# Performance work log

Hardware: AMD Instinct MI355X
Metric: run time of the kernel (lower is better)

## Reference

```python
import jax, jax.numpy as jnp
import numpy as np

B, T, D, H1, H2, O = 256, 200, 1250, 100, 20, 2
P = 0.2  # dropout prob (training=True in the original forward)


def setup_inputs() -> dict:
    key = jax.random.key(0)
    ks = jax.random.split(key, 13)
    s1 = 1.0 / np.sqrt(H1)  # torch nn.RNN init: U(-1/sqrt(hidden), 1/sqrt(hidden))
    s2 = 1.0 / np.sqrt(H2)
    sf = 1.0 / np.sqrt(H2)  # fc fan_in = 20
    u = lambda k, shape, s: jax.random.uniform(k, shape, jnp.float32, -s, s)
    keep = 1.0 - P
    return {
        "x": jax.random.normal(ks[0], (B, T, D), jnp.float32),
        "W_ih1": u(ks[1], (H1, D), s1),
        "W_hh1": u(ks[2], (H1, H1), s1),
        "b_ih1": u(ks[3], (H1,), s1),
        "b_hh1": u(ks[4], (H1,), s1),
        "W_ih2": u(ks[5], (H2, H1), s2),
        "W_hh2": u(ks[6], (H2, H2), s2),
        "b_ih2": u(ks[7], (H2,), s2),
        "b_hh2": u(ks[8], (H2,), s2),
        "W_fc": u(ks[9], (O, H2), sf),
        "b_fc": u(ks[10], (O,), sf),
        # pre-sampled inverted-dropout masks (training=True), scaled by 1/keep
        "mask1": jax.random.bernoulli(ks[11], keep, (B, T, H1)).astype(jnp.float32) / keep,
        "mask2": jax.random.bernoulli(ks[12], keep, (B, T, H2)).astype(jnp.float32) / keep,
    }


def _relu_rnn(x, W_ih, W_hh, b_ih, b_hh):
    # x: [B,T,Din] -> outputs [B,T,H]. Hoist the input projection out of the scan.
    pre = jnp.einsum("btd,hd->bth", x, W_ih) + b_ih + b_hh  # [B,T,H]
    h0 = jnp.zeros((x.shape[0], W_hh.shape[0]), x.dtype)

    def step(h, pre_t):
        h = jax.nn.relu(pre_t + h @ W_hh.T)
        return h, h

    _, out = jax.lax.scan(step, h0, jnp.swapaxes(pre, 0, 1))  # [T,B,H]
    return jnp.swapaxes(out, 0, 1)


def reference(x, W_ih1, W_hh1, b_ih1, b_hh1, W_ih2, W_hh2, b_ih2, b_hh2,
              W_fc, b_fc, mask1, mask2):
    out = _relu_rnn(x, W_ih1, W_hh1, b_ih1, b_hh1) * mask1          # rnn1 + dropout
    out = _relu_rnn(out, W_ih2, W_hh2, b_ih2, b_hh2) * mask2        # rnn2 + dropout
    return out[:, -1, :] @ W_fc.T + b_fc                            # fc on last step
```

## Files before the change

### kernel.cpp

```cpp
#include <hip/hip_runtime.h>

#define NB 256
#define TT 200
#define DD 1250
#define H1 100
#define H2 20
#define NO 2

#define BM 64
#define GRID_A (51200 / BM)
#define KC 64
#define NCH 20
#define WR 112
#define KPAD 1280

typedef __attribute__((ext_vector_type(4))) float f32x4;
typedef __attribute__((ext_vector_type(8))) short s16x8;

__device__ __forceinline__ unsigned short f2bf(float f) {
    unsigned u = __builtin_bit_cast(unsigned, f);
    u += 0x7FFFu + ((u >> 16) & 1u);
    return (unsigned short)(u >> 16);
}
__device__ __forceinline__ float bf2f(unsigned short s) {
    unsigned u = ((unsigned)s) << 16;
    return __builtin_bit_cast(float, u);
}

#define GLL(srcp, dstp) __builtin_amdgcn_global_load_lds( \
    (const __attribute__((address_space(1))) void*)(srcp), \
    (__attribute__((address_space(3))) void*)(dstp), 16, 0, 0)

__global__ void prep_w(const float* __restrict__ Wih1, unsigned short* __restrict__ w_ws)
{
    const int idx = blockIdx.x * 256 + threadIdx.x;
    if (idx >= WR * KPAD / 4) return;
    const int r  = idx / (KPAD / 4);
    const int k4 = (idx - r * (KPAD / 4)) * 4;
    unsigned short o[4];
    #pragma unroll
    for (int e = 0; e < 4; ++e) {
        const int k = k4 + e;
        o[e] = (r < H1 && k < DD) ? f2bf(Wih1[r * DD + k]) : (unsigned short)0;
    }
    uint2 pk;
    pk.x = (unsigned)o[0] | ((unsigned)o[1] << 16);
    pk.y = (unsigned)o[2] | ((unsigned)o[3] << 16);
    *(uint2*)&w_ws[r * KPAD + k4] = pk;
}

__launch_bounds__(256, 4)
__global__ void gemm_pre(const float* __restrict__ x,
                         const unsigned short* __restrict__ w_ws,
                         unsigned short* __restrict__ preT)
{
    __shared__ __align__(16) float          a_sf[2][BM * 64];
    __shared__ __align__(16) unsigned short w_sh[2][WR * 64];

    const int tid = threadIdx.x;
    const int bid = blockIdx.x;
    const int wv  = tid >> 6;
    const int ln  = tid & 63;
    const int c16 = ln & 15;
    const int kgrp = ln >> 4;

    f32x4 acc[7];
    #pragma unroll
    for (int i = 0; i < 7; ++i)
        #pragma unroll
        for (int c = 0; c < 4; ++c) acc[i][c] = 0.f;

    auto agll = [&](int k0, int buf) {
        #pragma unroll
        for (int q = 0; q < 4; ++q) {
            const int idx  = tid + q * 256;
            const int row  = idx >> 4;
            const int segp = idx & 15;
            const int segl = segp ^ (row & 15);
            const float* src = x + (size_t)(bid * BM + row) * DD + k0 + segl * 4;
            GLL(src, &a_sf[buf][idx * 4]);
        }
    };
    auto wgll = [&](int k0, int buf) {
        #pragma unroll
        for (int q = 0; q < 4; ++q) {
            const int idx = tid + q * 256;
            if (idx < WR * 8) {
                const int row = idx >> 3;
                const int c8p = idx & 7;
                const int c8l = c8p ^ (row & 7);
                const unsigned short* src = w_ws + row * KPAD + k0 + c8l * 8;
                GLL(src, &w_sh[buf][idx * 8]);
            }
        }
    };

    auto mfma_chunk = [&](int buf) {
        #pragma unroll
        for (int s = 0; s < 2; ++s) {
            const int row_a = wv * 16 + c16;
            const int sb = s * 8 + kgrp * 2;
            const int sp0 = (sb + 0) ^ (row_a & 15);
            const int sp1 = (sb + 1) ^ (row_a & 15);
            const float4 av0 = *(const float4*)&a_sf[buf][row_a * 64 + sp0 * 4];
            const float4 av1 = *(const float4*)&a_sf[buf][row_a * 64 + sp1 * 4];
            const s16x8 af = {
                (short)f2bf(av0.x), (short)f2bf(av0.y),
                (short)f2bf(av0.z), (short)f2bf(av0.w),
                (short)f2bf(av1.x), (short)f2bf(av1.y),
                (short)f2bf(av1.z), (short)f2bf(av1.w) };
            #pragma unroll
            for (int nt = 0; nt < 7; ++nt) {
                const int row_b = nt * 16 + c16;
                const int c8  = s * 4 + kgrp;
                const int c8p = c8 ^ (row_b & 7);
                const s16x8 bf = *(const s16x8*)&w_sh[buf][row_b * 64 + c8p * 8];
                acc[nt] = __builtin_amdgcn_mfma_f32_16x16x32_bf16(af, bf, acc[nt], 0, 0, 0);
            }
        }
    };

    float4 ta[4];
    #pragma unroll
    for (int q = 0; q < 4; ++q) {
        const int idx  = tid + q * 256;
        const int row  = idx >> 4;
        const int segl = idx & 15;
        const int gk   = 19 * KC + segl * 4;
        const float* xp = x + (size_t)(bid * BM + row) * DD + gk;
        float4 v;
        v.x = (gk + 0 < DD) ? xp[0] : 0.f;
        v.y = (gk + 1 < DD) ? xp[1] : 0.f;
        v.z = (gk + 2 < DD) ? xp[2] : 0.f;
        v.w = (gk + 3 < DD) ? xp[3] : 0.f;
        ta[q] = v;
    }

    agll(0, 0);
    wgll(0, 0);

    for (int kc = 0; kc < 19; ++kc) {
        const int buf = kc & 1;
        __syncthreads();
        if (kc + 1 < 19) agll((kc + 1) * KC, buf ^ 1);
        wgll((kc + 1) * KC, buf ^ 1);
        mfma_chunk(buf);
    }

    #pragma unroll
    for (int q = 0; q < 4; ++q) {
        const int idx  = tid + q * 256;
        const int row  = idx >> 4;
        const int segl = idx & 15;
        const int sp   = segl ^ (row & 15);
        *(float4*)&a_sf[1][row * 64 + sp * 4] = ta[q];
    }
    __syncthreads();
    mfma_chunk(1);

    const int rg = bid * BM + wv * 16 + (kgrp << 2);
    #pragma unroll
    for (int nt = 0; nt < 7; ++nt) {
        const int col = nt * 16 + c16;
        if (col < H1) {
            #pragma unroll
            for (int r = 0; r < 4; ++r)
                preT[(size_t)(rg + r) * H1 + col] = f2bf(acc[nt][r]);
        }
    }
}

#define FMA4(W, PTR) { const float4 hv_ = *(const float4*)(PTR);            \
    a0 = fmaf((W).x, hv_.x, a0); a1 = fmaf((W).y, hv_.y, a1);               \
    a2 = fmaf((W).z, hv_.z, a2); a3 = fmaf((W).w, hv_.w, a3); }

#define CH 8
#define NCHK 25

__launch_bounds__(320, 1)
__global__ void scan_rnn(const unsigned short* __restrict__ preT,
                         const float* __restrict__ Whh1,
                         const float* __restrict__ bih1,
                         const float* __restrict__ bhh1,
                         const float* __restrict__ Wih2,
                         const float* __restrict__ Whh2,
                         const float* __restrict__ bih2,
                         const float* __restrict__ bhh2,
                         const float* __restrict__ Wfc,
                         const float* __restrict__ bfc,
                         const float* __restrict__ mask1,
                         const float* __restrict__ mask2,
                         float* __restrict__ out)
{
    __shared__ alignas(16) float h1_s[2][104];
    __shared__ alignas(16) float c_s[2][120];
    __shared__ alignas(16) float h2f_s[H2];
    __shared__ alignas(16) float m_lds[2][CH * H1];
    __shared__ alignas(16) float p_lds[2][CH * H1];

    const int tid = threadIdx.x;
    const int b   = blockIdx.x;
    const float* m1b = mask1 + (size_t)b * TT * H1;
    const unsigned short* pTb = preT + (size_t)b * TT * H1;

    const int h = tid >> 1;
    const int p = tid & 1;
    const bool l1t = (tid < 200);
    const bool l2t = (tid >= 256 && tid < 256 + 2 * H2);
    const int k2 = (tid - 256) >> 1;
    const int p3 = (tid - 256) & 1;

    float4 w00{}, w01{}, w02{}, w03{}, w04{}, w05{}, w06{}, w07{},
           w08{}, w09{}, w10{}, w11{}, w12{}, w13{}, w14{};
    float b1 = 0.f, b2 = 0.f;

    if (l1t) {
        const float* wr = Whh1 + h * H1 + p * 52;
        w00 = *(const float4*)(wr +  0); w01 = *(const float4*)(wr +  4);
        w02 = *(const float4*)(wr +  8); w03 = *(const float4*)(wr + 12);
        w04 = *(const float4*)(wr + 16); w05 = *(const float4*)(wr + 20);
        w06 = *(const float4*)(wr + 24); w07 = *(const float4*)(wr + 28);
        w08 = *(const float4*)(wr + 32); w09 = *(const float4*)(wr + 36);
        w10 = *(const float4*)(wr + 40); w11 = *(const float4*)(wr + 44);
        if (p == 0) { w12 = *(const float4*)(wr + 48); b1 = bih1[h] + bhh1[h]; }
    } else if (l2t) {
        if (p3 == 0) {
            const float* wr = Wih2 + k2 * H1;
            w00 = *(const float4*)(wr +  0); w01 = *(const float4*)(wr +  4);
            w02 = *(const float4*)(wr +  8); w03 = *(const float4*)(wr + 12);
            w04 = *(const float4*)(wr + 16); w05 = *(const float4*)(wr + 20);
            w06 = *(const float4*)(wr + 24); w07 = *(const float4*)(wr + 28);
            w08 = *(const float4*)(wr + 32); w09 = *(const float4*)(wr + 36);
            w10 = *(const float4*)(wr + 40); w11 = *(const float4*)(wr + 44);
            w12 = *(const float4*)(wr + 48); w13 = *(const float4*)(wr + 52);
            w14 = *(const float4*)(wr + 56);
            b2 = bih2[k2] + bhh2[k2];
        } else {
            const float* wr = Wih2 + k2 * H1 + 60;
            w00 = *(const float4*)(wr +  0); w01 = *(const float4*)(wr +  4);
            w02 = *(const float4*)(wr +  8); w03 = *(const float4*)(wr + 12);
            w04 = *(const float4*)(wr + 16); w05 = *(const float4*)(wr + 20);
            w06 = *(const float4*)(wr + 24); w07 = *(const float4*)(wr + 28);
            w08 = *(const float4*)(wr + 32); w09 = *(const float4*)(wr + 36);
            const float* wh = Whh2 + k2 * H2;
            w10 = *(const float4*)(wh +  0); w11 = *(const float4*)(wh +  4);
            w12 = *(const float4*)(wh +  8); w13 = *(const float4*)(wh + 12);
            w14 = *(const float4*)(wh + 16);
        }
    }

    for (int i = tid; i < 104; i += 320) { h1_s[0][i] = 0.f; h1_s[1][i] = 0.f; }
    for (int i = tid; i < 120; i += 320) { c_s[0][i] = 0.f; c_s[1][i] = 0.f; }

    if (tid < 200) {
        const float4 mv = *(const float4*)&m1b[tid * 4];
        *(float4*)&m_lds[0][tid * 4] = mv;
    } else if (tid < 300) {
        const s16x8 pv = *(const s16x8*)&pTb[(tid - 200) * 8];
        float* dst = &p_lds[0][(tid - 200) * 8];
        *(float4*)dst       = make_float4(bf2f(pv[0]), bf2f(pv[1]), bf2f(pv[2]), bf2f(pv[3]));
        *(float4*)(dst + 4) = make_float4(bf2f(pv[4]), bf2f(pv[5]), bf2f(pv[6]), bf2f(pv[7]));
    }
    __syncthreads();

    int buf = 0;
    for (int c = 0; c < NCHK; ++c) {
        const bool more = (c + 1 < NCHK);
        float4 mst{}; s16x8 pst{};

        #pragma unroll
        for (int u = 0; u < CH; ++u) {
            const int t = c * CH + u;
            const int cur = t & 1, nxt = cur ^ 1;

            if (u > 0) __syncthreads();

            if (u == 0 && more) {
                const int base = (c + 1) * (CH * H1);
                if (tid < 200)      mst = *(const float4*)&m1b[base + tid * 4];
                else if (tid < 300) pst = *(const s16x8*)&pTb[base + (tid - 200) * 8];
            }

            if (l1t) {
                float a0 = (p == 0) ? (p_lds[buf][u * H1 + h] + b1) : 0.f;
                const float mv = (p == 1) ? m_lds[buf][u * H1 + h] : 0.f;
                float a1 = 0.f, a2 = 0.f, a3 = 0.f;
                const float* hb = &h1_s[cur][p * 52];
                FMA4(w00, hb +  0); FMA4(w01, hb +  4); FMA4(w02, hb +  8);
                FMA4(w03, hb + 12); FMA4(w04, hb + 16); FMA4(w05, hb + 20);
                FMA4(w06, hb + 24); FMA4(w07, hb + 28); FMA4(w08, hb + 32);
                FMA4(w09, hb + 36); FMA4(w10, hb + 40); FMA4(w11, hb + 44);
                FMA4(w12, hb + 48);
                float part = (a0 + a1) + (a2 + a3);
                float tot  = part + __shfl_xor(part, 1);
                tot = fmaxf(tot, 0.f);
                if (p == 0) h1_s[nxt][h] = tot;
                else        c_s[nxt][h] = tot * mv;
            }

            if (l2t && t >= 1) {
                float a0 = (p3 == 0) ? b2 : 0.f;
                float a1 = 0.f, a2 = 0.f, a3 = 0.f;
                const float* cb = &c_s[cur][p3 * 60];
                FMA4(w00, cb +  0); FMA4(w01, cb +  4); FMA4(w02, cb +  8);
                FMA4(w03, cb + 12); FMA4(w04, cb + 16); FMA4(w05, cb + 20);
                FMA4(w06, cb + 24); FMA4(w07, cb + 28); FMA4(w08, cb + 32);
                FMA4(w09, cb + 36); FMA4(w10, cb + 40); FMA4(w11, cb + 44);
                FMA4(w12, cb + 48); FMA4(w13, cb + 52); FMA4(w14, cb + 56);
                float part = (a0 + a1) + (a2 + a3);
                part += __shfl_xor(part, 1);
                const float h2v = fmaxf(part, 0.f);
                if (p3 == 0) c_s[nxt][100 + k2] = h2v;
            }
        }

        if (more) {
            if (tid < 200) {
                *(float4*)&m_lds[buf ^ 1][tid * 4] = mst;
            } else if (tid < 300) {
                float* dst = &p_lds[buf ^ 1][(tid - 200) * 8];
                *(float4*)dst       = make_float4(bf2f(pst[0]), bf2f(pst[1]), bf2f(pst[2]), bf2f(pst[3]));
                *(float4*)(dst + 4) = make_float4(bf2f(pst[4]), bf2f(pst[5]), bf2f(pst[6]), bf2f(pst[7]));
            }
            buf ^= 1;
        }
        __syncthreads();
    }

    {
        const int cur = TT & 1;
        if (l2t) {
            float a0 = (p3 == 0) ? b2 : 0.f;
            float a1 = 0.f, a2 = 0.f, a3 = 0.f;
            const float* cb = &c_s[cur][p3 * 60];
            FMA4(w00, cb +  0); FMA4(w01, cb +  4); FMA4(w02, cb +  8);
            FMA4(w03, cb + 12); FMA4(w04, cb + 16); FMA4(w05, cb + 20);
            FMA4(w06, cb + 24); FMA4(w07, cb + 28); FMA4(w08, cb + 32);
            FMA4(w09, cb + 36); FMA4(w10, cb + 40); FMA4(w11, cb + 44);
            FMA4(w12, cb + 48); FMA4(w13, cb + 52); FMA4(w14, cb + 56);
            float part = (a0 + a1) + (a2 + a3);
            part += __shfl_xor(part, 1);
            if (p3 == 0) h2f_s[k2] = fmaxf(part, 0.f);
        }
        __syncthreads();
    }

    if (tid < NO) {
        const float* m2 = mask2 + ((size_t)b * TT + (TT - 1)) * H2;
        float s = bfc[tid];
        #pragma unroll
        for (int k = 0; k < H2; ++k)
            s = fmaf(Wfc[tid * H2 + k], h2f_s[k] * m2[k], s);
        out[b * NO + tid] = s;
    }
}

extern "C" void kernel_launch(void* const* d_in, const int* in_sizes, int n_in,
                              void* d_out, int out_size, void* d_ws, size_t ws_size,
                              hipStream_t stream) {
    const float* x     = (const float*)d_in[0];
    const float* Wih1  = (const float*)d_in[1];
    const float* Whh1  = (const float*)d_in[2];
    const float* bih1  = (const float*)d_in[3];
    const float* bhh1  = (const float*)d_in[4];
    const float* Wih2  = (const float*)d_in[5];
    const float* Whh2  = (const float*)d_in[6];
    const float* bih2  = (const float*)d_in[7];
    const float* bhh2  = (const float*)d_in[8];
    const float* Wfc   = (const float*)d_in[9];
    const float* bfc   = (const float*)d_in[10];
    const float* mask1 = (const float*)d_in[11];
    const float* mask2 = (const float*)d_in[12];
    float* out = (float*)d_out;

    unsigned short* preT = (unsigned short*)d_ws;
    unsigned short* w_ws = (unsigned short*)((char*)d_ws + 10240000);

    prep_w  <<<dim3((WR * KPAD / 4 + 255) / 256), dim3(256), 0, stream>>>(Wih1, w_ws);
    gemm_pre<<<dim3(GRID_A), dim3(256), 0, stream>>>(x, w_ws, preT);
    scan_rnn<<<dim3(NB), dim3(320), 0, stream>>>(preT, Whh1, bih1, bhh1,
                                                 Wih2, Whh2, bih2, bhh2,
                                                 Wfc, bfc, mask1, mask2, out);
}
```

Baseline: 169.5 us.

## Process two batch rows per scan block to halve grid and share barriers

The scan kernel now handles two batch elements per workgroup. The register-resident recurrent weights are reused for both sequences, and each step's barrier covers twice the work. The grid shrinks from 256 to 128 blocks, so the blocks fit within the device's compute units and each block amortises its sync latency over two independent recurrences. In exchange, each step does twice the serial FMA work per thread, which lengthens the per-step critical path.

```diff
diff --git a/kernel.cpp b/kernel.cpp
--- a/kernel.cpp
+++ b/kernel.cpp
@@ -192,16 +192,18 @@
                          const float* __restrict__ mask2,
                          float* __restrict__ out)
 {
-    __shared__ alignas(16) float h1_s[2][104];
-    __shared__ alignas(16) float c_s[2][120];
-    __shared__ alignas(16) float h2f_s[H2];
-    __shared__ alignas(16) float m_lds[2][CH * H1];
-    __shared__ alignas(16) float p_lds[2][CH * H1];
+    __shared__ alignas(16) float h1_s[2][2][104];
+    __shared__ alignas(16) float c_s[2][2][120];
+    __shared__ alignas(16) float h2f_s[2][H2];
+    __shared__ alignas(16) float m_lds[2][2][CH * H1];
+    __shared__ alignas(16) float p_lds[2][2][CH * H1];
 
     const int tid = threadIdx.x;
-    const int b   = blockIdx.x;
-    const float* m1b = mask1 + (size_t)b * TT * H1;
-    const unsigned short* pTb = preT + (size_t)b * TT * H1;
+    const int b0  = blockIdx.x * 2;
+    const float* m1b[2] = { mask1 + (size_t)(b0 + 0) * TT * H1,
+                            mask1 + (size_t)(b0 + 1) * TT * H1 };
+    const unsigned short* pTb[2] = { preT + (size_t)(b0 + 0) * TT * H1,
+                                     preT + (size_t)(b0 + 1) * TT * H1 };
 
     const int h = tid >> 1;
     const int p = tid & 1;
@@ -249,24 +251,33 @@
         }
     }
 
-    for (int i = tid; i < 104; i += 320) { h1_s[0][i] = 0.f; h1_s[1][i] = 0.f; }
-    for (int i = tid; i < 120; i += 320) { c_s[0][i] = 0.f; c_s[1][i] = 0.f; }
+    for (int i = tid; i < 104; i += 320) {
+        h1_s[0][0][i] = 0.f; h1_s[0][1][i] = 0.f;
+        h1_s[1][0][i] = 0.f; h1_s[1][1][i] = 0.f;
+    }
+    for (int i = tid; i < 120; i += 320) {
+        c_s[0][0][i] = 0.f; c_s[0][1][i] = 0.f;
+        c_s[1][0][i] = 0.f; c_s[1][1][i] = 0.f;
+    }
 
     if (tid < 200) {
-        const float4 mv = *(const float4*)&m1b[tid * 4];
-        *(float4*)&m_lds[0][tid * 4] = mv;
+        *(float4*)&m_lds[0][0][tid * 4] = *(const float4*)&m1b[0][tid * 4];
+        *(float4*)&m_lds[1][0][tid * 4] = *(const float4*)&m1b[1][tid * 4];
     } else if (tid < 300) {
-        const s16x8 pv = *(const s16x8*)&pTb[(tid - 200) * 8];
-        float* dst = &p_lds[0][(tid - 200) * 8];
-        *(float4*)dst       = make_float4(bf2f(pv[0]), bf2f(pv[1]), bf2f(pv[2]), bf2f(pv[3]));
-        *(float4*)(dst + 4) = make_float4(bf2f(pv[4]), bf2f(pv[5]), bf2f(pv[6]), bf2f(pv[7]));
+        #pragma unroll
+        for (int bb = 0; bb < 2; ++bb) {
+            const s16x8 pv = *(const s16x8*)&pTb[bb][(tid - 200) * 8];
+            float* dst = &p_lds[bb][0][(tid - 200) * 8];
+            *(float4*)dst       = make_float4(bf2f(pv[0]), bf2f(pv[1]), bf2f(pv[2]), bf2f(pv[3]));
+            *(float4*)(dst + 4) = make_float4(bf2f(pv[4]), bf2f(pv[5]), bf2f(pv[6]), bf2f(pv[7]));
+        }
     }
     __syncthreads();
 
     int buf = 0;
     for (int c = 0; c < NCHK; ++c) {
         const bool more = (c + 1 < NCHK);
-        float4 mst{}; s16x8 pst{};
+        float4 mstA{}, mstB{}; s16x8 pstA{}, pstB{};
 
         #pragma unroll
         for (int u = 0; u < CH; ++u) {
@@ -277,31 +288,79 @@
 
             if (u == 0 && more) {
                 const int base = (c + 1) * (CH * H1);
-                if (tid < 200)      mst = *(const float4*)&m1b[base + tid * 4];
-                else if (tid < 300) pst = *(const s16x8*)&pTb[base + (tid - 200) * 8];
+                if (tid < 200) {
+                    mstA = *(const float4*)&m1b[0][base + tid * 4];
+                    mstB = *(const float4*)&m1b[1][base + tid * 4];
+                } else if (tid < 300) {
+                    pstA = *(const s16x8*)&pTb[0][base + (tid - 200) * 8];
+                    pstB = *(const s16x8*)&pTb[1][base + (tid - 200) * 8];
+                }
             }
 
             if (l1t) {
-                float a0 = (p == 0) ? (p_lds[buf][u * H1 + h] + b1) : 0.f;
-                const float mv = (p == 1) ? m_lds[buf][u * H1 + h] : 0.f;
-                float a1 = 0.f, a2 = 0.f, a3 = 0.f;
-                const float* hb = &h1_s[cur][p * 52];
-                FMA4(w00, hb +  0); FMA4(w01, hb +  4); FMA4(w02, hb +  8);
-                FMA4(w03, hb + 12); FMA4(w04, hb + 16); FMA4(w05, hb + 20);
-                FMA4(w06, hb + 24); FMA4(w07, hb + 28); FMA4(w08, hb + 32);
-                FMA4(w09, hb + 36); FMA4(w10, hb + 40); FMA4(w11, hb + 44);
-                FMA4(w12, hb + 48);
-                float part = (a0 + a1) + (a2 + a3);
-                float tot  = part + __shfl_xor(part, 1);
-                tot = fmaxf(tot, 0.f);
-                if (p == 0) h1_s[nxt][h] = tot;
-                else        c_s[nxt][h] = tot * mv;
+                #pragma unroll
+                for (int bb = 0; bb < 2; ++bb) {
+                    float a0 = (p == 0) ? (p_lds[bb][buf][u * H1 + h] + b1) : 0.f;
+                    const float mv = (p == 1) ? m_lds[bb][buf][u * H1 + h] : 0.f;
+                    float a1 = 0.f, a2 = 0.f, a3 = 0.f;
+                    const float* hb = &h1_s[bb][cur][p * 52];
+                    FMA4(w00, hb +  0); FMA4(w01, hb +  4); FMA4(w02, hb +  8);
+                    FMA4(w03, hb + 12); FMA4(w04, hb + 16); FMA4(w05, hb + 20);
+                    FMA4(w06, hb + 24); FMA4(w07, hb + 28); FMA4(w08, hb + 32);
+                    FMA4(w09, hb + 36); FMA4(w10, hb + 40); FMA4(w11, hb + 44);
+                    FMA4(w12, hb + 48);
+                    float part = (a0 + a1) + (a2 + a3);
+                    float tot  = part + __shfl_xor(part, 1);
+                    tot = fmaxf(tot, 0.f);
+                    if (p == 0) h1_s[bb][nxt][h] = tot;
+                    else        c_s[bb][nxt][h] = tot * mv;
+                }
             }
 
             if (l2t && t >= 1) {
+                #pragma unroll
+                for (int bb = 0; bb < 2; ++bb) {
+                    float a0 = (p3 == 0) ? b2 : 0.f;
+                    float a1 = 0.f, a2 = 0.f, a3 = 0.f;
+                    const float* cb = &c_s[bb][cur][p3 * 60];
+                    FMA4(w00, cb +  0); FMA4(w01, cb +  4); FMA4(w02, cb +  8);
+                    FMA4(w03, cb + 12); FMA4(w04, cb + 16); FMA4(w05, cb + 20);
+                    FMA4(w06, cb + 24); FMA4(w07, cb + 28); FMA4(w08, cb + 32);
+                    FMA4(w09, cb + 36); FMA4(w10, cb + 40); FMA4(w11, cb + 44);
+                    FMA4(w12, cb + 48); FMA4(w13, cb + 52); FMA4(w14, cb + 56);
+                    float part = (a0 + a1) + (a2 + a3);
+                    part += __shfl_xor(part, 1);
+                    const float h2v = fmaxf(part, 0.f);
+                    if (p3 == 0) c_s[bb][nxt][100 + k2] = h2v;
+                }
+            }
+        }
+
+        if (more) {
+            if (tid < 200) {
+                *(float4*)&m_lds[0][buf ^ 1][tid * 4] = mstA;
+                *(float4*)&m_lds[1][buf ^ 1][tid * 4] = mstB;
+            } else if (tid < 300) {
+                float* dA = &p_lds[0][buf ^ 1][(tid - 200) * 8];
+                *(float4*)dA       = make_float4(bf2f(pstA[0]), bf2f(pstA[1]), bf2f(pstA[2]), bf2f(pstA[3]));
+                *(float4*)(dA + 4) = make_float4(bf2f(pstA[4]), bf2f(pstA[5]), bf2f(pstA[6]), bf2f(pstA[7]));
+                float* dB = &p_lds[1][buf ^ 1][(tid - 200) * 8];
+                *(float4*)dB       = make_float4(bf2f(pstB[0]), bf2f(pstB[1]), bf2f(pstB[2]), bf2f(pstB[3]));
+                *(float4*)(dB + 4) = make_float4(bf2f(pstB[4]), bf2f(pstB[5]), bf2f(pstB[6]), bf2f(pstB[7]));
+            }
+            buf ^= 1;
+        }
+        __syncthreads();
+    }
+
+    {
+        const int cur = TT & 1;
+        if (l2t) {
+            #pragma unroll
+            for (int bb = 0; bb < 2; ++bb) {
                 float a0 = (p3 == 0) ? b2 : 0.f;
                 float a1 = 0.f, a2 = 0.f, a3 = 0.f;
-                const float* cb = &c_s[cur][p3 * 60];
+                const float* cb = &c_s[bb][cur][p3 * 60];
                 FMA4(w00, cb +  0); FMA4(w01, cb +  4); FMA4(w02, cb +  8);
                 FMA4(w03, cb + 12); FMA4(w04, cb + 16); FMA4(w05, cb + 20);
                 FMA4(w06, cb + 24); FMA4(w07, cb + 28); FMA4(w08, cb + 32);
@@ -309,49 +368,21 @@
                 FMA4(w12, cb + 48); FMA4(w13, cb + 52); FMA4(w14, cb + 56);
                 float part = (a0 + a1) + (a2 + a3);
                 part += __shfl_xor(part, 1);
-                const float h2v = fmaxf(part, 0.f);
-                if (p3 == 0) c_s[nxt][100 + k2] = h2v;
-            }
-        }
-
-        if (more) {
-            if (tid < 200) {
-                *(float4*)&m_lds[buf ^ 1][tid * 4] = mst;
-            } else if (tid < 300) {
-                float* dst = &p_lds[buf ^ 1][(tid - 200) * 8];
-                *(float4*)dst       = make_float4(bf2f(pst[0]), bf2f(pst[1]), bf2f(pst[2]), bf2f(pst[3]));
-                *(float4*)(dst + 4) = make_float4(bf2f(pst[4]), bf2f(pst[5]), bf2f(pst[6]), bf2f(pst[7]));
-            }
-            buf ^= 1;
+                if (p3 == 0) h2f_s[bb][k2] = fmaxf(part, 0.f);
+            }
         }
         __syncthreads();
     }
 
-    {
-        const int cur = TT & 1;
-        if (l2t) {
-            float a0 = (p3 == 0) ? b2 : 0.f;
-            float a1 = 0.f, a2 = 0.f, a3 = 0.f;
-            const float* cb = &c_s[cur][p3 * 60];
-            FMA4(w00, cb +  0); FMA4(w01, cb +  4); FMA4(w02, cb +  8);
-            FMA4(w03, cb + 12); FMA4(w04, cb + 16); FMA4(w05, cb + 20);
-            FMA4(w06, cb + 24); FMA4(w07, cb + 28); FMA4(w08, cb + 32);
-            FMA4(w09, cb + 36); FMA4(w10, cb + 40); FMA4(w11, cb + 44);
-            FMA4(w12, cb + 48); FMA4(w13, cb + 52); FMA4(w14, cb + 56);
-            float part = (a0 + a1) + (a2 + a3);
-            part += __shfl_xor(part, 1);
-            if (p3 == 0) h2f_s[k2] = fmaxf(part, 0.f);
-        }
-        __syncthreads();
-    }
-
-    if (tid < NO) {
-        const float* m2 = mask2 + ((size_t)b * TT + (TT - 1)) * H2;
-        float s = bfc[tid];
+    if (tid < 2 * NO) {
+        const int bb = tid >> 1;
+        const int o  = tid & 1;
+        const float* m2 = mask2 + ((size_t)(b0 + bb) * TT + (TT - 1)) * H2;
+        float s = bfc[o];
         #pragma unroll
         for (int k = 0; k < H2; ++k)
-            s = fmaf(Wfc[tid * H2 + k], h2f_s[k] * m2[k], s);
-        out[b * NO + tid] = s;
+            s = fmaf(Wfc[o * H2 + k], h2f_s[bb][k] * m2[k], s);
+        out[(b0 + bb) * NO + o] = s;
     }
 }
 
@@ -378,7 +409,7 @@
 
     prep_w  <<<dim3((WR * KPAD / 4 + 255) / 256), dim3(256), 0, stream>>>(Wih1, w_ws);
     gemm_pre<<<dim3(GRID_A), dim3(256), 0, stream>>>(x, w_ws, preT);
-    scan_rnn<<<dim3(NB), dim3(320), 0, stream>>>(preT, Whh1, bih1, bhh1,
-                                                 Wih2, Whh2, bih2, bhh2,
-                                                 Wfc, bfc, mask1, mask2, out);
-}
+    scan_rnn<<<dim3(NB / 2), dim3(320), 0, stream>>>(preT, Whh1, bih1, bhh1,
+                                                     Wih2, Whh2, bih2, bhh2,
+                                                     Wfc, bfc, mask1, mask2, out);
+}
```

Result: slower. 237.6 us (+40.2%).
